# Kernel optimization log

Hardware: AMD Instinct MI355X
Metric: run time of the kernel (lower is better)

The kernel has to match this reference:

```python
import jax, jax.numpy as jnp
import numpy as np

N = 100000      # nodes
E = 3200000     # edges
F_IN = 78       # num_features_mol
F_GAT = 256     # mol_out_feats
HEADS = 2
F_HYP = 128     # mol_out_feats_hyper


def setup_inputs() -> dict:
    key = jax.random.key(0)
    ks = jax.random.split(key, 32)
    g = lambda k, s: jax.random.normal(k, s, dtype=jnp.float32) * 0.05
    inp = {}
    inp["mol_x"] = jax.random.normal(ks[0], (N, F_IN), dtype=jnp.float32)
    inp["mol_edge_index"] = jax.random.randint(ks[1], (2, E), 0, N)
    inp["hyper_edge"] = jax.random.randint(ks[2], (2, E), 0, N)
    # GAT layer 1 (78 -> 256, 2 heads, concat=False)
    inp["W1"] = g(ks[3], (F_IN, HEADS * F_GAT)); inp["as1"] = g(ks[4], (HEADS, F_GAT)); inp["ad1"] = g(ks[5], (HEADS, F_GAT)); inp["b1"] = jnp.zeros((F_GAT,), jnp.float32)
    # GAT layers 2,3 (256 -> 256)
    inp["W2"] = g(ks[6], (F_GAT, HEADS * F_GAT)); inp["as2"] = g(ks[7], (HEADS, F_GAT)); inp["ad2"] = g(ks[8], (HEADS, F_GAT)); inp["b2"] = jnp.zeros((F_GAT,), jnp.float32)
    inp["W3"] = g(ks[9], (F_GAT, HEADS * F_GAT)); inp["as3"] = g(ks[10], (HEADS, F_GAT)); inp["ad3"] = g(ks[11], (HEADS, F_GAT)); inp["b3"] = jnp.zeros((F_GAT,), jnp.float32)
    # GRU-style gating fusion
    inp["fc1_w"] = g(ks[12], (F_GAT, F_GAT)); inp["fc1_b"] = jnp.zeros((F_GAT,), jnp.float32)
    inp["fc2_w"] = g(ks[13], (F_GAT, F_GAT)); inp["fc2_b"] = jnp.zeros((F_GAT,), jnp.float32)
    inp["mol_bias"] = jax.random.uniform(ks[14], (1, F_GAT), jnp.float32, -0.2, 0.2)
    # HypergraphConv layers (334 -> 128 -> 128)
    inp["theta1"] = g(ks[15], (F_GAT + F_IN, F_HYP)); inp["hb1"] = jnp.zeros((F_HYP,), jnp.float32)
    inp["theta2"] = g(ks[16], (F_HYP, F_HYP)); inp["hb2"] = jnp.zeros((F_HYP,), jnp.float32)
    return inp


def _gat(x, src, dst, W, a_s, a_d, b):
    # PyG GATConv, heads=2, concat=False, eval mode (no dropout), self-loops pre-added in src/dst
    xh = (x @ W).reshape(N, HEADS, F_GAT)            # [N,H,C]
    a_src = (xh * a_s).sum(-1)                        # [N,H]
    a_dst = (xh * a_d).sum(-1)                        # [N,H]
    e = jax.nn.leaky_relu(a_src[src] + a_dst[dst], 0.2)  # [E',H]
    m = jax.ops.segment_max(e, dst, num_segments=N)
    ex = jnp.exp(e - m[dst])
    s = jax.ops.segment_sum(ex, dst, num_segments=N)
    alpha = ex / s[dst]                               # softmax over incoming edges
    out = jax.ops.segment_sum(xh[src] * alpha[:, :, None], dst, num_segments=N)
    return out.mean(axis=1) + b                       # concat=False -> head mean


def _hyper(x, node, edge, theta, b):
    # PyG HypergraphConv, use_attention=False: D^-1 H B^-1 H^T X Theta + b
    xt = x @ theta
    ones = jnp.ones((node.shape[0],), xt.dtype)
    D = jax.ops.segment_sum(ones, node, num_segments=N)
    B = jax.ops.segment_sum(ones, edge, num_segments=N)
    Dinv = jnp.where(D > 0, 1.0 / D, 0.0)
    Binv = jnp.where(B > 0, 1.0 / B, 0.0)
    ef = Binv[:, None] * jax.ops.segment_sum(xt[node], edge, num_segments=N)
    nf = Dinv[:, None] * jax.ops.segment_sum(ef[edge], node, num_segments=N)
    return nf + b


def _forward(mol_x, mol_edge_index, hyper_edge,
             W1, as1, ad1, b1, W2, as2, ad2, b2, W3, as3, ad3, b3,
             fc1_w, fc1_b, fc2_w, fc2_b, mol_bias, theta1, hb1, theta2, hb2):
    loops = jnp.arange(N, dtype=mol_edge_index.dtype)
    src = jnp.concatenate([mol_edge_index[0], loops])
    dst = jnp.concatenate([mol_edge_index[1], loops])
    hyper_x0 = jax.lax.stop_gradient(mol_x)  # .clone().detach()
    # layer 0
    h = jax.nn.relu(_gat(mol_x, src, dst, W1, as1, ad1, b1))
    # layer 1 (relu) + gate
    x = jax.nn.relu(_gat(h, src, dst, W2, as2, ad2, b2))
    z = jax.nn.sigmoid(x @ fc1_w.T + fc1_b + h @ fc2_w.T + fc2_b + mol_bias)
    h = z * x + (1.0 - z) * h
    # layer 2 (no relu) + gate
    x = _gat(h, src, dst, W3, as3, ad3, b3)
    z = jax.nn.sigmoid(x @ fc1_w.T + fc1_b + h @ fc2_w.T + fc2_b + mol_bias)
    h = z * x + (1.0 - z) * h
    # hypergraph branch (source uses mol_edge_index here, hyper_edge is unused)
    hx = jnp.concatenate([jax.lax.stop_gradient(h), hyper_x0], axis=1)
    node, edge = mol_edge_index[0], mol_edge_index[1]
    hx = jax.nn.relu(_hyper(hx, node, edge, theta1, hb1))
    hx = jax.nn.relu(_hyper(hx, node, edge, theta2, hb2))
    return jnp.concatenate([h, hx], axis=1)  # [N, 384]


def reference(mol_x, mol_edge_index, hyper_edge,
              W1, as1, ad1, b1, W2, as2, ad2, b2, W3, as3, ad3, b3,
              fc1_w, fc1_b, fc2_w, fc2_b, mol_bias, theta1, hb1, theta2, hb2):
    return _forward(mol_x, mol_edge_index, hyper_edge,
                    W1, as1, ad1, b1, W2, as2, ad2, b2, W3, as3, ad3, b3,
                    fc1_w, fc1_b, fc2_w, fc2_b, mol_bias, theta1, hb1, theta2, hb2)
```

## Files before the change

### kernel.cpp

```cpp
#include <hip/hip_runtime.h>

typedef unsigned short u16;
typedef __attribute__((ext_vector_type(8))) short short8v;
typedef __attribute__((ext_vector_type(8))) unsigned short ushort8v;
typedef __attribute__((ext_vector_type(4))) unsigned short ushort4v;
typedef __attribute__((ext_vector_type(4))) float f32x4;
typedef __attribute__((ext_vector_type(2))) float f32x2;

__device__ __forceinline__ float bf2f(u16 u) {
    union { unsigned int i; float f; } v; v.i = ((unsigned int)u) << 16; return v.f;
}
__device__ __forceinline__ u16 f2bf(float f) {
    union { float f; unsigned int i; } v; v.f = f;
    unsigned int i = v.i;
    return (u16)((i + 0x7FFFu + ((i >> 16) & 1u)) >> 16);
}
__device__ __forceinline__ float leaky02(float x) { return x > 0.f ? x : 0.2f * x; }
__device__ __forceinline__ float load_in(const void* p, long i, int isbf) {
    return isbf ? bf2f(((const u16*)p)[i]) : ((const float*)p)[i];
}
__device__ __forceinline__ f32x2 pk_fma(f32x2 a, f32x2 b, f32x2 c) {
    f32x2 d;
    asm("v_pk_fma_f32 %0, %1, %2, %3" : "=v"(d) : "v"(a), "v"(b), "v"(c));
    return d;
}
__device__ __forceinline__ f32x2 pk_add(f32x2 a, f32x2 b) {
    f32x2 d;
    asm("v_pk_add_f32 %0, %1, %2" : "=v"(d) : "v"(a), "v"(b));
    return d;
}
__device__ __forceinline__ f32x2 bfpair(unsigned int d) {
    union { unsigned int i; float f; } lo, hi;
    lo.i = d << 16;
    hi.i = d & 0xFFFF0000u;
    f32x2 r; r.x = lo.f; r.y = hi.f; return r;
}
__device__ __forceinline__ float bperm_f(int addr, float v) {
    return __int_as_float(__builtin_amdgcn_ds_bpermute(addr, __float_as_int(v)));
}
__device__ __forceinline__ int bperm_i(int addr, int v) {
    return __builtin_amdgcn_ds_bpermute(addr, v);
}

__global__ void detect_kernel(const unsigned* __restrict__ w, int* __restrict__ flag) {
    __shared__ int cnt;
    int t = threadIdx.x;
    if (t == 0) cnt = 0;
    __syncthreads();
    unsigned x = w[t * 16];
    unsigned lo = x & 0xFFFFu;
    int e = (int)((x >> 7) & 0xFFu);
    int good = (lo == 0u) || (e >= 100 && e <= 140);
    atomicAdd(&cnt, good);
    __syncthreads();
    if (t == 0) *flag = (cnt > 128) ? 1 : 0;
}

#define CSR_NBK 1024

__global__ __launch_bounds__(256)
void bucket_count_kernel(const int* __restrict__ ei, int* __restrict__ bcs,
                         int* __restrict__ bcd, int E_, int n, int SH) {
    __shared__ int hs[CSR_NBK], hd[CSR_NBK];
    const int t = threadIdx.x;
    for (int i = t; i < CSR_NBK; i += 256) { hs[i] = 0; hd[i] = 0; }
    __syncthreads();
    const int e0 = blockIdx.x * 4096;
    #pragma unroll
    for (int k = 0; k < 16; ++k) {
        int e = e0 + k * 256 + t;
        if (e < E_) {
            int s = ei[e], d = ei[E_ + e];
            if ((unsigned)s >= (unsigned)n) s = 0;
            if ((unsigned)d >= (unsigned)n) d = 0;
            atomicAdd(&hs[s >> SH], 1);
            atomicAdd(&hd[d >> SH], 1);
        }
    }
    __syncthreads();
    for (int i = t; i < CSR_NBK; i += 256) {
        if (hs[i]) atomicAdd(&bcs[i], hs[i]);
        if (hd[i]) atomicAdd(&bcd[i], hd[i]);
    }
}

__global__ void scan_excl_kernel(const int* __restrict__ deg, int* __restrict__ ptr, int n) {
    __shared__ int s_woff[17];
    __shared__ int s_carry;
    const int t = threadIdx.x;
    const int lane = t & 63, wid = t >> 6;
    if (t == 0) s_carry = 0;
    __syncthreads();
    for (int base = 0; base < n; base += 1024) {
        int i = base + t;
        int v = (i < n) ? deg[i] : 0;
        int incl = v;
        #pragma unroll
        for (int d = 1; d < 64; d <<= 1) {
            int x = __shfl_up(incl, d, 64);
            if (lane >= d) incl += x;
        }
        if (lane == 63) s_woff[wid] = incl;
        __syncthreads();
        if (t == 0) {
            int run = 0;
            #pragma unroll
            for (int w = 0; w < 16; ++w) { int x = s_woff[w]; s_woff[w] = run; run += x; }
            s_woff[16] = run;
        }
        __syncthreads();
        int excl = s_carry + s_woff[wid] + incl - v;
        if (i < n) ptr[i] = excl;
        __syncthreads();
        if (t == 0) s_carry += s_woff[16];
        __syncthreads();
    }
    if (t == 0) ptr[n] = s_carry;
}

__global__ void copy2_kernel(const int* __restrict__ a, int* __restrict__ b,
                             const int* __restrict__ c, int* __restrict__ d2, int n) {
    int i = blockIdx.x * 256 + threadIdx.x;
    if (i < n) { b[i] = a[i]; d2[i] = c[i]; }
}

__global__ __launch_bounds__(256)
void partition_kernel(const int* __restrict__ ei, int* __restrict__ bcur_s,
                      int* __restrict__ bcur_d, int2* __restrict__ ps,
                      int2* __restrict__ pd, int E_, int n, int SH) {
    __shared__ int cs[CSR_NBK], cd[CSR_NBK], bs[CSR_NBK], bd[CSR_NBK];
    const int t = threadIdx.x;
    for (int i = t; i < CSR_NBK; i += 256) { cs[i] = 0; cd[i] = 0; }
    __syncthreads();
    const int e0 = blockIdx.x * 4096;
    int sv[16], dv[16];
    #pragma unroll
    for (int k = 0; k < 16; ++k) {
        int e = e0 + k * 256 + t;
        int s = -1, d = 0;
        if (e < E_) {
            s = ei[e]; d = ei[E_ + e];
            if ((unsigned)s >= (unsigned)n) s = 0;
            if ((unsigned)d >= (unsigned)n) d = 0;
            atomicAdd(&cs[s >> SH], 1);
            atomicAdd(&cd[d >> SH], 1);
        }
        sv[k] = (e < E_) ? s : -1;
        dv[k] = d;
    }
    __syncthreads();
    for (int i = t; i < CSR_NBK; i += 256) {
        bs[i] = cs[i] ? atomicAdd(&bcur_s[i], cs[i]) : 0;
        bd[i] = cd[i] ? atomicAdd(&bcur_d[i], cd[i]) : 0;
        cs[i] = 0; cd[i] = 0;
    }
    __syncthreads();
    #pragma unroll
    for (int k = 0; k < 16; ++k) {
        int s = sv[k];
        if (s < 0) continue;
        int d = dv[k];
        int p = bs[s >> SH] + atomicAdd(&cs[s >> SH], 1);
        ps[p] = make_int2(d, s);
        int q = bd[d >> SH] + atomicAdd(&cd[d >> SH], 1);
        pd[q] = make_int2(s, d);
    }
}

__global__ __launch_bounds__(256)
void fill_bucket_kernel(const int2* __restrict__ pairs, const int* __restrict__ bptr,
                        int* __restrict__ ptr, int* __restrict__ idx, int n, int SH) {
    __shared__ int cnt[256];
    __shared__ int wsum[5];
    const int b = blockIdx.x;
    const int n0 = b << SH;
    if (n0 >= n) return;
    const int nn = min(1 << SH, n - n0);
    const int t = threadIdx.x;
    cnt[t] = 0;
    __syncthreads();
    const int pbeg = bptr[b], pend = bptr[b + 1];
    for (int j = pbeg + t; j < pend; j += 256)
        atomicAdd(&cnt[pairs[j].y - n0], 1);
    __syncthreads();
    const int c = (t < nn) ? cnt[t] : 0;
    int v = c;
    const int lane = t & 63, wid = t >> 6;
    #pragma unroll
    for (int d = 1; d < 64; d <<= 1) {
        int x = __shfl_up(v, d, 64);
        if (lane >= d) v += x;
    }
    if (lane == 63) wsum[wid] = v;
    __syncthreads();
    if (t == 0) {
        int r = 0;
        #pragma unroll
        for (int w = 0; w < 4; ++w) { int x = wsum[w]; wsum[w] = r; r += x; }
        wsum[4] = r;
    }
    __syncthreads();
    v += wsum[wid];
    const int excl = pbeg + v - c;
    __syncthreads();
    if (t < nn) { cnt[t] = excl; ptr[n0 + t] = excl; }
    if (t == 0 && n0 + nn == n) ptr[n] = pbeg + wsum[4];
    __syncthreads();
    for (int j = pbeg + t; j < pend; j += 256) {
        int2 pr = pairs[j];
        int p = atomicAdd(&cnt[pr.y - n0], 1);
        idx[p] = pr.x;
    }
}

__global__ void ingest_transpose_kernel(const void* __restrict__ src, long base,
                                        u16* __restrict__ dst, int K, int Nc, int Kp,
                                        const int* __restrict__ flag) {
    int i = blockIdx.x * 256 + threadIdx.x;
    if (i >= Nc * Kp) return;
    int n = i / Kp, k = i - n * Kp;
    float v = (k < K) ? load_in(src, base + (long)k * Nc + n, *flag) : 0.f;
    dst[i] = f2bf(v);
}

__global__ void ingest_copy_kernel(const void* __restrict__ src, u16* __restrict__ dst,
                                   int n, const int* __restrict__ flag) {
    int i = blockIdx.x * 256 + threadIdx.x;
    if (i < n) dst[i] = f2bf(load_in(src, i, *flag));
}

__global__ void ingest_wcat_kernel(const void* __restrict__ W, u16* __restrict__ dst,
                                   int Kin, int Fh, const int* __restrict__ flag) {
    int i = blockIdx.x * 256 + threadIdx.x;
    int tot = 256 * 2 * Fh;
    if (i >= tot) return;
    int o = i / (2 * Fh), k = i - o * 2 * Fh;
    int h = k / Fh, c = k - h * Fh;
    float v = (c < Kin) ? 0.5f * load_in(W, (long)c * 512 + h * 256 + o, *flag) : 0.f;
    dst[i] = f2bf(v);
}

__global__ void ingest_bcat_kernel(const void* __restrict__ fc1, const void* __restrict__ fc2,
                                   u16* __restrict__ dst, const int* __restrict__ flag) {
    int i = blockIdx.x * 256 + threadIdx.x;
    if (i >= 256 * 512) return;
    int o = i >> 9, k = i & 511;
    float v = (k < 256) ? load_in(fc1, (long)o * 256 + k, *flag)
                        : load_in(fc2, (long)o * 256 + k - 256, *flag);
    dst[i] = f2bf(v);
}

__global__ void ingest_pad_molx_kernel(const void* __restrict__ x, u16* __restrict__ dst,
                                       int ldd, int total, const int* __restrict__ flag) {
    int i = blockIdx.x * 256 + threadIdx.x;
    if (i >= total) return;
    int r = i / 96, c = i - r * 96;
    float v = (c < 78) ? load_in(x, (long)r * 78 + c, *flag) : 0.f;
    dst[(size_t)r * ldd + c] = f2bf(v);
}

__global__ void attn_vec_kernel(const void* __restrict__ W, const void* __restrict__ as_,
                                const void* __restrict__ ad_, float* __restrict__ was,
                                float* __restrict__ wad, int Kin, int Fh,
                                const int* __restrict__ flag) {
    int i = blockIdx.x * 256 + threadIdx.x;
    if (i >= 2 * Fh) return;
    int h = i / Fh, c = i - h * Fh;
    float s = 0.f, d = 0.f;
    if (c < Kin) {
        int f = *flag;
        for (int o = 0; o < 256; ++o) {
            float w = load_in(W, (long)c * 512 + h * 256 + o, f);
            s += w * load_in(as_, h * 256 + o, f);
            d += w * load_in(ad_, h * 256 + o, f);
        }
    }
    was[i] = s; wad[i] = d;
}

__global__ __launch_bounds__(256, 2)
void gemm_kernel(const u16* __restrict__ A, int lda,
                 const u16* __restrict__ Bt, int ldb,
                 u16* __restrict__ C, int ldc, int K, int M, int beta,
                 const u16* __restrict__ bias, int relu) {
    __shared__ __align__(16) u16 As[128 * 32];
    __shared__ __align__(16) u16 Bs[128 * 32];
    const int tid = threadIdx.x;
    const int wave = tid >> 6, lane = tid & 63;
    const int m0 = blockIdx.x * 128;
    const int n0 = blockIdx.y * 128;
    const int wm = (wave & 1) * 64, wn = (wave >> 1) * 64;
    const int r = lane & 15, q = lane >> 4;

    f32x4 acc[4][4];
    if (beta) {
        #pragma unroll
        for (int i = 0; i < 4; ++i)
            #pragma unroll
            for (int j = 0; j < 4; ++j)
                #pragma unroll
                for (int rr = 0; rr < 4; ++rr) {
                    size_t gr = (size_t)(m0 + wm + 16 * i + q * 4 + rr);
                    int gc = n0 + wn + 16 * j + r;
                    acc[i][j][rr] = bf2f(C[gr * ldc + gc]);
                }
    } else {
        #pragma unroll
        for (int i = 0; i < 4; ++i)
            #pragma unroll
            for (int j = 0; j < 4; ++j) acc[i][j] = (f32x4)0.f;
    }

    const int rowT = wave * 16 + (lane >> 2);
    const int koff = (lane & 3) * 8;
    int rA0 = m0 + rowT;       if (rA0 > M - 1) rA0 = M - 1;
    int rA1 = m0 + rowT + 64;  if (rA1 > M - 1) rA1 = M - 1;
    const u16* gA0 = A + (size_t)rA0 * lda + koff;
    const u16* gA1 = A + (size_t)rA1 * lda + koff;
    const u16* gB0 = Bt + (size_t)(n0 + rowT) * ldb + koff;
    const u16* gB1 = Bt + (size_t)(n0 + rowT + 64) * ldb + koff;
    u16* sA0 = &As[rowT * 32 + koff];
    u16* sA1 = &As[(rowT + 64) * 32 + koff];
    u16* sB0 = &Bs[rowT * 32 + koff];
    u16* sB1 = &Bs[(rowT + 64) * 32 + koff];

    const int nK = K >> 5;
    for (int kt = 0; kt < nK; ++kt) {
        ushort8v ta0 = *(const ushort8v*)gA0;
        ushort8v ta1 = *(const ushort8v*)gA1;
        ushort8v tb0 = *(const ushort8v*)gB0;
        ushort8v tb1 = *(const ushort8v*)gB1;
        gA0 += 32; gA1 += 32; gB0 += 32; gB1 += 32;
        __syncthreads();
        *(ushort8v*)sA0 = ta0;
        *(ushort8v*)sA1 = ta1;
        *(ushort8v*)sB0 = tb0;
        *(ushort8v*)sB1 = tb1;
        __syncthreads();
        short8v af[4], bf[4];
        #pragma unroll
        for (int i = 0; i < 4; ++i) af[i] = *(const short8v*)&As[(wm + 16 * i + r) * 32 + q * 8];
        #pragma unroll
        for (int j = 0; j < 4; ++j) bf[j] = *(const short8v*)&Bs[(wn + 16 * j + r) * 32 + q * 8];
        #pragma unroll
        for (int i = 0; i < 4; ++i)
            #pragma unroll
            for (int j = 0; j < 4; ++j)
                acc[i][j] = __builtin_amdgcn_mfma_f32_16x16x32_bf16(af[i], bf[j], acc[i][j], 0, 0, 0);
    }
    #pragma unroll
    for (int j = 0; j < 4; ++j) {
        int gc = n0 + wn + 16 * j + r;
        float bv = bias ? bf2f(bias[gc]) : 0.f;
        #pragma unroll
        for (int i = 0; i < 4; ++i)
            #pragma unroll
            for (int rr = 0; rr < 4; ++rr) {
                size_t gr = (size_t)(m0 + wm + 16 * i + q * 4 + rr);
                float x = acc[i][j][rr] + bv;
                if (relu) x = fmaxf(x, 0.f);
                C[gr * ldc + gc] = f2bf(x);
            }
    }
}

__global__ __launch_bounds__(256)
void attn_dots_h_kernel(const u16* __restrict__ hsrc, int ldh,
                        const float* __restrict__ was, const float* __restrict__ wad,
                        float* __restrict__ a_src, float* __restrict__ a_dst,
                        int Fh, int n) {
    int v = blockIdx.x * 4 + (threadIdx.x >> 6);
    if (v >= n) return;
    const int lane = threadIdx.x & 63;
    const int c0 = lane * 4;
    float ps0 = 0.f, pd0 = 0.f, ps1 = 0.f, pd1 = 0.f;
    if (c0 < Fh) {
        ushort4v xv = *(const ushort4v*)&hsrc[(size_t)v * ldh + c0];
        #pragma unroll
        for (int k = 0; k < 4; ++k) {
            float x = bf2f(xv[k]);
            ps0 += x * was[c0 + k];
            pd0 += x * wad[c0 + k];
            ps1 += x * was[Fh + c0 + k];
            pd1 += x * wad[Fh + c0 + k];
        }
    }
    #pragma unroll
    for (int d = 1; d < 64; d <<= 1) {
        ps0 += __shfl_xor(ps0, d, 64); pd0 += __shfl_xor(pd0, d, 64);
        ps1 += __shfl_xor(ps1, d, 64); pd1 += __shfl_xor(pd1, d, 64);
    }
    if (lane == 0) {
        a_src[2 * v] = ps0; a_src[2 * v + 1] = ps1;
        a_dst[2 * v] = pd0; a_dst[2 * v + 1] = pd1;
    }
}

template <int NG>
__global__ __launch_bounds__(256)
void gat_agg_h_kernel(const u16* __restrict__ hsrc, int ldh, int F,
                      const float* __restrict__ asrc, const float* __restrict__ adst,
                      const int* __restrict__ ptr, const int* __restrict__ idx,
                      u16* __restrict__ agg, int ldagg, int n, int Etot) {
    constexpr int GL = 64 / NG;
    int v = blockIdx.x * 4 + (threadIdx.x >> 6);
    if (v >= n) return;
    const int lane = threadIdx.x & 63;
    const int sub = lane / GL;
    const int c0 = (lane & (GL - 1)) * 8;
    const int act = (c0 < F);
    int beg = ptr[v], end = ptr[v + 1];
    beg = min(max(beg, 0), Etot);
    end = min(max(end, beg), Etot);
    const float ad0 = adst[2 * v], ad1 = adst[2 * v + 1];
    const float es0 = leaky02(asrc[2 * v] + ad0);
    const float es1 = leaky02(asrc[2 * v + 1] + ad1);
    float m0 = es0, m1 = es1;
    float s0 = 0.f, s1 = 0.f;
    f32x2 f0p[4], f1p[4];
    #pragma unroll
    for (int p = 0; p < 4; ++p) { f0p[p] = (f32x2)0.f; f1p[p] = (f32x2)0.f; }

    for (int cb = beg; cb < end; cb += 64) {
        const int cnt = min(64, end - cb);
        int sE = 0;
        float sc0 = -1e30f, sc1 = -1e30f;
        if (lane < cnt) {
            sE = idx[cb + lane];
            sE = ((unsigned)sE < (unsigned)n) ? sE : 0;
            sc0 = leaky02(asrc[2 * sE] + ad0);
            sc1 = leaky02(asrc[2 * sE + 1] + ad1);
        }
        float cm0 = sc0, cm1 = sc1;
        #pragma unroll
        for (int d = 1; d < 64; d <<= 1) {
            cm0 = fmaxf(cm0, __shfl_xor(cm0, d, 64));
            cm1 = fmaxf(cm1, __shfl_xor(cm1, d, 64));
        }
        const float nm0 = fmaxf(m0, cm0), nm1 = fmaxf(m1, cm1);
        const float r0 = __expf(m0 - nm0), r1 = __expf(m1 - nm1);
        m0 = nm0; m1 = nm1;
        s0 *= r0; s1 *= r1;
        #pragma unroll
        for (int p = 0; p < 4; ++p) {
            f0p[p].x *= r0; f0p[p].y *= r0;
            f1p[p].x *= r1; f1p[p].y *= r1;
        }
        float wE0 = 0.f, wE1 = 0.f;
        if (lane < cnt) {
            wE0 = __expf(sc0 - m0);
            wE1 = __expf(sc1 - m1);
            s0 += wE0; s1 += wE1;
        }
        const int nIt = (cnt + 4 * NG - 1) / (4 * NG);
        int jj = sub;
        for (int it = 0; it < nIt; ++it, jj += 4 * NG) {
            const int aA = jj * 4, aB = aA + NG * 4, aC = aA + NG * 8, aD = aA + NG * 12;
            const int sA = bperm_i(aA, sE);
            const int sB = bperm_i(aB, sE);
            const int sC = bperm_i(aC, sE);
            const int sD = bperm_i(aD, sE);
            const float wA0 = bperm_f(aA, wE0), wA1 = bperm_f(aA, wE1);
            const float wB0 = bperm_f(aB, wE0), wB1 = bperm_f(aB, wE1);
            const float wC0 = bperm_f(aC, wE0), wC1 = bperm_f(aC, wE1);
            const float wD0 = bperm_f(aD, wE0), wD1 = bperm_f(aD, wE1);
            if (act) {
                const uint4 fA = *(const uint4*)&hsrc[(size_t)sA * ldh + c0];
                const uint4 fB = *(const uint4*)&hsrc[(size_t)sB * ldh + c0];
                const uint4 fC = *(const uint4*)&hsrc[(size_t)sC * ldh + c0];
                const uint4 fD = *(const uint4*)&hsrc[(size_t)sD * ldh + c0];
                const f32x2 wA0v = {wA0, wA0}, wA1v = {wA1, wA1};
                const f32x2 wB0v = {wB0, wB0}, wB1v = {wB1, wB1};
                const f32x2 wC0v = {wC0, wC0}, wC1v = {wC1, wC1};
                const f32x2 wD0v = {wD0, wD0}, wD1v = {wD1, wD1};
                #pragma unroll
                for (int p = 0; p < 4; ++p) {
                    const f32x2 xA = bfpair(((const unsigned*)&fA)[p]);
                    const f32x2 xB = bfpair(((const unsigned*)&fB)[p]);
                    const f32x2 xC = bfpair(((const unsigned*)&fC)[p]);
                    const f32x2 xD = bfpair(((const unsigned*)&fD)[p]);
                    f0p[p] = pk_fma(xA, wA0v, f0p[p]);
                    f1p[p] = pk_fma(xA, wA1v, f1p[p]);
                    f0p[p] = pk_fma(xB, wB0v, f0p[p]);
                    f1p[p] = pk_fma(xB, wB1v, f1p[p]);
                    f0p[p] = pk_fma(xC, wC0v, f0p[p]);
                    f1p[p] = pk_fma(xC, wC1v, f1p[p]);
                    f0p[p] = pk_fma(xD, wD0v, f0p[p]);
                    f1p[p] = pk_fma(xD, wD1v, f1p[p]);
                }
            }
        }
    }
    #pragma unroll
    for (int d = 1; d < 64; d <<= 1) {
        s0 += __shfl_xor(s0, d, 64);
        s1 += __shfl_xor(s1, d, 64);
    }
    const float w0s = __expf(es0 - m0), w1s = __expf(es1 - m1);
    s0 += w0s; s1 += w1s;
    if (sub == 0 && act) {
        const uint4 f = *(const uint4*)&hsrc[(size_t)v * ldh + c0];
        const f32x2 w0v = {w0s, w0s}, w1v = {w1s, w1s};
        #pragma unroll
        for (int p = 0; p < 4; ++p) {
            const f32x2 x = bfpair(((const unsigned*)&f)[p]);
            f0p[p] = pk_fma(x, w0v, f0p[p]);
            f1p[p] = pk_fma(x, w1v, f1p[p]);
        }
    }
    #pragma unroll
    for (int p = 0; p < 4; ++p) {
        #pragma unroll
        for (int d = GL; d < 64; d <<= 1) {
            f0p[p].x += __shfl_xor(f0p[p].x, d, 64);
            f0p[p].y += __shfl_xor(f0p[p].y, d, 64);
            f1p[p].x += __shfl_xor(f1p[p].x, d, 64);
            f1p[p].y += __shfl_xor(f1p[p].y, d, 64);
        }
    }
    if (lane < GL && act) {
        const float i0 = 1.f / s0, i1 = 1.f / s1;
        ushort8v o0, o1;
        #pragma unroll
        for (int p = 0; p < 4; ++p) {
            o0[2 * p] = f2bf(f0p[p].x * i0); o0[2 * p + 1] = f2bf(f0p[p].y * i0);
            o1[2 * p] = f2bf(f1p[p].x * i1); o1[2 * p + 1] = f2bf(f1p[p].y * i1);
        }
        *(ushort8v*)&agg[(size_t)v * ldagg + c0] = o0;
        *(ushort8v*)&agg[(size_t)v * ldagg + F + c0] = o1;
    }
}

__global__ __launch_bounds__(256)
void gate_kernel(const u16* __restrict__ logit, const u16* __restrict__ cat,
                 const u16* __restrict__ fc1b, const u16* __restrict__ fc2b,
                 const u16* __restrict__ molb, u16* __restrict__ dest,
                 void* __restrict__ outw, const int* __restrict__ flag, int n) {
    int i = blockIdx.x * 256 + threadIdx.x;
    if (i >= n) return;
    int node = i >> 5, c0 = (i & 31) * 8;
    ushort8v lg = *(const ushort8v*)&logit[(size_t)node * 256 + c0];
    ushort8v xv = *(const ushort8v*)&cat[(size_t)node * 512 + c0];
    ushort8v hv = *(const ushort8v*)&cat[(size_t)node * 512 + 256 + c0];
    ushort8v b1v = *(const ushort8v*)&fc1b[c0];
    ushort8v b2v = *(const ushort8v*)&fc2b[c0];
    ushort8v mbv = *(const ushort8v*)&molb[c0];
    float ov[8];
    ushort8v dv;
    #pragma unroll
    for (int k = 0; k < 8; ++k) {
        float l = bf2f(lg[k]) + bf2f(b1v[k]) + bf2f(b2v[k]) + bf2f(mbv[k]);
        float z = 1.f / (1.f + __expf(-l));
        ov[k] = z * bf2f(xv[k]) + (1.f - z) * bf2f(hv[k]);
        dv[k] = f2bf(ov[k]);
    }
    *(ushort8v*)&dest[(size_t)node * 512 + c0] = dv;
    if (outw) {
        if (*flag) {
            *(ushort8v*)((u16*)outw + (size_t)node * 384 + c0) = dv;
        } else {
            float* o = (float*)outw + (size_t)node * 384 + c0;
            #pragma unroll
            for (int k = 0; k < 8; ++k) o[k] = ov[k];
        }
    }
}

__global__ __launch_bounds__(256)
void hyper_gather_kernel(const u16* __restrict__ feat, const int* __restrict__ ptr,
                         const int* __restrict__ idx, const u16* __restrict__ bias,
                         u16* __restrict__ outb, int ldo, void* __restrict__ outw,
                         int col0, const int* __restrict__ flag,
                         int do_relu, int n, int Etot) {
    int v = blockIdx.x * 4 + (threadIdx.x >> 6);
    if (v >= n) return;
    const int lane = threadIdx.x & 63;
    const int c0 = (lane & 15) * 8, sub = lane >> 4;
    int beg = ptr[v], end = ptr[v + 1];
    beg = min(max(beg, 0), Etot);
    end = min(max(end, beg), Etot);
    const float inv = (end > beg) ? 1.f / (float)(end - beg) : 0.f;
    f32x2 a2[4];
    #pragma unroll
    for (int p = 0; p < 4; ++p) a2[p] = (f32x2)0.f;
    int j = beg + sub;
    for (; j + 12 < end; j += 16) {
        int sA = idx[j];      sA = ((unsigned)sA < (unsigned)n) ? sA : 0;
        int sB = idx[j + 4];  sB = ((unsigned)sB < (unsigned)n) ? sB : 0;
        int sC = idx[j + 8];  sC = ((unsigned)sC < (unsigned)n) ? sC : 0;
        int sD = idx[j + 12]; sD = ((unsigned)sD < (unsigned)n) ? sD : 0;
        const uint4 fA = *(const uint4*)&feat[(size_t)sA * 128 + c0];
        const uint4 fB = *(const uint4*)&feat[(size_t)sB * 128 + c0];
        const uint4 fC = *(const uint4*)&feat[(size_t)sC * 128 + c0];
        const uint4 fD = *(const uint4*)&feat[(size_t)sD * 128 + c0];
        #pragma unroll
        for (int p = 0; p < 4; ++p) {
            a2[p] = pk_add(a2[p], bfpair(((const unsigned*)&fA)[p]));
            a2[p] = pk_add(a2[p], bfpair(((const unsigned*)&fB)[p]));
            a2[p] = pk_add(a2[p], bfpair(((const unsigned*)&fC)[p]));
            a2[p] = pk_add(a2[p], bfpair(((const unsigned*)&fD)[p]));
        }
    }
    for (; j < end; j += 4) {
        int s = idx[j]; s = ((unsigned)s < (unsigned)n) ? s : 0;
        const uint4 f = *(const uint4*)&feat[(size_t)s * 128 + c0];
        #pragma unroll
        for (int p = 0; p < 4; ++p)
            a2[p] = pk_add(a2[p], bfpair(((const unsigned*)&f)[p]));
    }
    #pragma unroll
    for (int p = 0; p < 4; ++p) {
        a2[p].x += __shfl_xor(a2[p].x, 16, 64);
        a2[p].y += __shfl_xor(a2[p].y, 16, 64);
        a2[p].x += __shfl_xor(a2[p].x, 32, 64);
        a2[p].y += __shfl_xor(a2[p].y, 32, 64);
    }
    if (sub == 0) {
        float ov[8];
        ushort8v o;
        #pragma unroll
        for (int p = 0; p < 4; ++p) {
            float x0 = a2[p].x * inv + (bias ? bf2f(bias[c0 + 2 * p]) : 0.f);
            float x1 = a2[p].y * inv + (bias ? bf2f(bias[c0 + 2 * p + 1]) : 0.f);
            if (do_relu) { x0 = fmaxf(x0, 0.f); x1 = fmaxf(x1, 0.f); }
            ov[2 * p] = x0; ov[2 * p + 1] = x1;
            o[2 * p] = f2bf(x0); o[2 * p + 1] = f2bf(x1);
        }
        if (outb) *(ushort8v*)&outb[(size_t)v * ldo + c0] = o;
        if (outw) {
            if (*flag) {
                *(ushort8v*)((u16*)outw + (size_t)v * 384 + col0 + c0) = o;
            } else {
                float* ofp = (float*)outw + (size_t)v * 384 + col0 + c0;
                #pragma unroll
                for (int k = 0; k < 8; ++k) ofp[k] = ov[k];
            }
        }
    }
}

extern "C" void kernel_launch(void* const* d_in, const int* in_sizes, int n_in,
                              void* d_out, int out_size, void* d_ws, size_t ws_size,
                              hipStream_t stream) {
    const void* molx = d_in[0];
    const int*  ei   = (const int*)d_in[1];
    const void* W1 = d_in[3], *as1 = d_in[4], *ad1 = d_in[5], *b1 = d_in[6];
    const void* W2 = d_in[7], *as2 = d_in[8], *ad2 = d_in[9], *b2 = d_in[10];
    const void* W3 = d_in[11], *as3 = d_in[12], *ad3 = d_in[13], *b3 = d_in[14];
    const void* fc1w = d_in[15], *fc1b = d_in[16], *fc2w = d_in[17], *fc2b = d_in[18];
    const void* molb = d_in[19];
    const void* th1 = d_in[20], *hb1 = d_in[21], *th2 = d_in[22], *hb2 = d_in[23];
    (void)n_in; (void)out_size;

    const int N = in_sizes[0] / 78;
    const int E = in_sizes[1] / 2;
    const int Mp = ((N + 127) / 128) * 128;

    int SH = 0;
    while (((N - 1) >> SH) >= CSR_NBK) SH++;

    char* base = (char*)d_ws;
    size_t off = 0;
    auto alloc = [&](size_t bytes) -> void* {
        void* r = base + off;
        off = (off + bytes + 255) & ~(size_t)255;
        return r;
    };
    int* flag = (int*)alloc(4);
    u16* bv1 = (u16*)alloc(256 * 2); u16* bv2 = (u16*)alloc(256 * 2); u16* bv3 = (u16*)alloc(256 * 2);
    u16* fc1bv = (u16*)alloc(256 * 2); u16* fc2bv = (u16*)alloc(256 * 2); u16* molbv = (u16*)alloc(256 * 2);
    u16* hb1v = (u16*)alloc(128 * 2); u16* hb2v = (u16*)alloc(128 * 2);
    float* was1 = (float*)alloc(192 * 4); float* wad1 = (float*)alloc(192 * 4);
    float* was2 = (float*)alloc(512 * 4); float* wad2 = (float*)alloc(512 * 4);
    float* was3 = (float*)alloc(512 * 4); float* wad3 = (float*)alloc(512 * 4);
    u16* Wc1 = (u16*)alloc(256 * 192 * 2);
    u16* Wc2 = (u16*)alloc(256 * 512 * 2);
    u16* Wc3 = (u16*)alloc(256 * 512 * 2);
    u16* Bcat = (u16*)alloc(256 * 512 * 2);
    u16* th1ta = (u16*)alloc(128 * 256 * 2);
    u16* th1tb = (u16*)alloc(128 * 96 * 2);
    u16* th2t  = (u16*)alloc(128 * 128 * 2);
    float* a_src = (float*)alloc((size_t)N * 2 * 4);
    float* a_dst = (float*)alloc((size_t)N * 2 * 4);
    int* ptr_src = (int*)alloc((size_t)(N + 1) * 4);
    int* ptr_dst = (int*)alloc((size_t)(N + 1) * 4);
    int* bcnt_src = (int*)alloc(CSR_NBK * 4);
    int* bcnt_dst = (int*)alloc(CSR_NBK * 4);
    int* bptr_src = (int*)alloc((CSR_NBK + 1) * 4);
    int* bptr_dst = (int*)alloc((CSR_NBK + 1) * 4);
    int* bcur_src = (int*)alloc(CSR_NBK * 4);
    int* bcur_dst = (int*)alloc(CSR_NBK * 4);
    int* idx_src = (int*)alloc((size_t)E * 4);
    int* idx_dst = (int*)alloc((size_t)E * 4);
    u16* cat = (u16*)alloc((size_t)Mp * 512 * 2);
    u16* agg = (u16*)alloc((size_t)Mp * 512 * 2);
    u16* xt   = agg;
    u16* efb  = agg + (size_t)Mp * 128;
    u16* hx1  = agg + (size_t)Mp * 256;
    u16* mxp2 = agg + (size_t)Mp * 384;

    int2* pairs_src; int2* pairs_dst;
    if (off + (size_t)E * 16 + 1024 <= ws_size) {
        pairs_src = (int2*)alloc((size_t)E * 8);
        pairs_dst = (int2*)alloc((size_t)E * 8);
    } else {
        pairs_src = (int2*)agg;
        pairs_dst = (int2*)((char*)agg + (size_t)E * 8);
    }

    const int nodeBlocks = (N + 3) / 4;
    const int eTiles = (E + 4095) / 4096;

    detect_kernel<<<1, 256, 0, stream>>>((const unsigned*)molx, flag);

    hipMemsetAsync(bcnt_src, 0, CSR_NBK * 4, stream);
    hipMemsetAsync(bcnt_dst, 0, CSR_NBK * 4, stream);
    bucket_count_kernel<<<eTiles, 256, 0, stream>>>(ei, bcnt_src, bcnt_dst, E, N, SH);
    scan_excl_kernel<<<1, 1024, 0, stream>>>(bcnt_src, bptr_src, CSR_NBK);
    scan_excl_kernel<<<1, 1024, 0, stream>>>(bcnt_dst, bptr_dst, CSR_NBK);
    copy2_kernel<<<(CSR_NBK + 255) / 256, 256, 0, stream>>>(bptr_src, bcur_src, bptr_dst, bcur_dst, CSR_NBK);
    partition_kernel<<<eTiles, 256, 0, stream>>>(ei, bcur_src, bcur_dst,
                                                 pairs_src, pairs_dst, E, N, SH);
    fill_bucket_kernel<<<CSR_NBK, 256, 0, stream>>>(pairs_src, bptr_src, ptr_src, idx_src, N, SH);
    fill_bucket_kernel<<<CSR_NBK, 256, 0, stream>>>(pairs_dst, bptr_dst, ptr_dst, idx_dst, N, SH);

    ingest_wcat_kernel<<<(256 * 192 + 255) / 256, 256, 0, stream>>>(W1, Wc1, 78, 96, flag);
    ingest_wcat_kernel<<<(256 * 512 + 255) / 256, 256, 0, stream>>>(W2, Wc2, 256, 256, flag);
    ingest_wcat_kernel<<<(256 * 512 + 255) / 256, 256, 0, stream>>>(W3, Wc3, 256, 256, flag);
    ingest_bcat_kernel<<<(256 * 512 + 255) / 256, 256, 0, stream>>>(fc1w, fc2w, Bcat, flag);
    ingest_transpose_kernel<<<(128 * 256 + 255) / 256, 256, 0, stream>>>(th1, 0, th1ta, 256, 128, 256, flag);
    ingest_transpose_kernel<<<(128 * 96 + 255) / 256, 256, 0, stream>>>(th1, (long)256 * 128, th1tb, 78, 128, 96, flag);
    ingest_transpose_kernel<<<(128 * 128 + 255) / 256, 256, 0, stream>>>(th2, 0, th2t, 128, 128, 128, flag);
    attn_vec_kernel<<<1, 256, 0, stream>>>(W1, as1, ad1, was1, wad1, 78, 96, flag);
    attn_vec_kernel<<<2, 256, 0, stream>>>(W2, as2, ad2, was2, wad2, 256, 256, flag);
    attn_vec_kernel<<<2, 256, 0, stream>>>(W3, as3, ad3, was3, wad3, 256, 256, flag);
    ingest_copy_kernel<<<1, 256, 0, stream>>>(b1, bv1, 256, flag);
    ingest_copy_kernel<<<1, 256, 0, stream>>>(b2, bv2, 256, flag);
    ingest_copy_kernel<<<1, 256, 0, stream>>>(b3, bv3, 256, flag);
    ingest_copy_kernel<<<1, 256, 0, stream>>>(fc1b, fc1bv, 256, flag);
    ingest_copy_kernel<<<1, 256, 0, stream>>>(fc2b, fc2bv, 256, flag);
    ingest_copy_kernel<<<1, 256, 0, stream>>>(molb, molbv, 256, flag);
    ingest_copy_kernel<<<1, 128, 0, stream>>>(hb1, hb1v, 128, flag);
    ingest_copy_kernel<<<1, 128, 0, stream>>>(hb2, hb2v, 128, flag);
    ingest_pad_molx_kernel<<<(N * 96 + 255) / 256, 256, 0, stream>>>(molx, cat, 512, N * 96, flag);

    auto gemm = [&](const u16* A, int lda, const u16* Bt, int ldb, u16* C, int ldc,
                    int K, int Nc, int M, int beta, const u16* bias, int relu) {
        dim3 g(Mp / 128, Nc / 128);
        gemm_kernel<<<g, 256, 0, stream>>>(A, lda, Bt, ldb, C, ldc, K, M, beta, bias, relu);
    };

    attn_dots_h_kernel<<<nodeBlocks, 256, 0, stream>>>(cat, 512, was1, wad1, a_src, a_dst, 96, N);
    gat_agg_h_kernel<4><<<nodeBlocks, 256, 0, stream>>>(cat, 512, 96, a_src, a_dst,
                                                        ptr_dst, idx_dst, agg, 192, N, E);
    gemm(agg, 192, Wc1, 192, cat + 256, 512, 192, 256, Mp, 0, bv1, 1);
    attn_dots_h_kernel<<<nodeBlocks, 256, 0, stream>>>(cat + 256, 512, was2, wad2, a_src, a_dst, 256, N);
    gat_agg_h_kernel<2><<<nodeBlocks, 256, 0, stream>>>(cat + 256, 512, 256, a_src, a_dst,
                                                        ptr_dst, idx_dst, agg, 512, N, E);
    gemm(agg, 512, Wc2, 512, cat, 512, 512, 256, Mp, 0, bv2, 1);
    gemm(cat, 512, Bcat, 512, agg , 256, 512, 256, Mp, 0, nullptr, 0);
    gate_kernel<<<(N * 32 + 255) / 256, 256, 0, stream>>>(agg, cat, fc1bv, fc2bv, molbv,
                                                          cat + 256, nullptr, flag, N * 32);
    attn_dots_h_kernel<<<nodeBlocks, 256, 0, stream>>>(cat + 256, 512, was3, wad3, a_src, a_dst, 256, N);
    gat_agg_h_kernel<2><<<nodeBlocks, 256, 0, stream>>>(cat + 256, 512, 256, a_src, a_dst,
                                                        ptr_dst, idx_dst, agg, 512, N, E);
    gemm(agg, 512, Wc3, 512, cat, 512, 512, 256, Mp, 0, bv3, 0);
    gemm(cat, 512, Bcat, 512, agg , 256, 512, 256, Mp, 0, nullptr, 0);
    gate_kernel<<<(N * 32 + 255) / 256, 256, 0, stream>>>(agg, cat, fc1bv, fc2bv, molbv,
                                                          cat + 256, d_out, flag, N * 32);
    ingest_pad_molx_kernel<<<(N * 96 + 255) / 256, 256, 0, stream>>>(molx, mxp2, 96, N * 96, flag);
    gemm(cat + 256, 512, th1ta, 256, xt, 128, 256, 128, Mp, 0, nullptr, 0);
    gemm(mxp2, 96, th1tb, 96, xt, 128, 96, 128, Mp, 1, nullptr, 0);
    hyper_gather_kernel<<<nodeBlocks, 256, 0, stream>>>(xt, ptr_dst, idx_dst, (const u16*)nullptr,
                                                        efb, 128, nullptr, 0, flag, 0, N, E);
    hyper_gather_kernel<<<nodeBlocks, 256, 0, stream>>>(efb, ptr_src, idx_src, hb1v,
                                                        hx1, 128, nullptr, 0, flag, 1, N, E);
    gemm(hx1, 128, th2t, 128, xt, 128, 128, 128, Mp, 0, nullptr, 0);
    hyper_gather_kernel<<<nodeBlocks, 256, 0, stream>>>(xt, ptr_dst, idx_dst, (const u16*)nullptr,
                                                        efb, 128, nullptr, 0, flag, 0, N, E);
    hyper_gather_kernel<<<nodeBlocks, 256, 0, stream>>>(efb, ptr_src, idx_src, hb2v,
                                                        (u16*)nullptr, 0, d_out, 256, flag, 1, N, E);
}
```

Measured before the change: 2.128 ms.

## Drop online-max softmax in GAT aggregation, use direct global-to-LDS GEMM loads

The GAT aggregation kernel drops the chunked online-softmax and its wave-wide max reductions and bpermute broadcasts. Each lane group now loads its own edge indices and computes exp weights directly, with scores clamped at 80 so the exponential cannot overflow. The GEMM stages tiles through global_load_lds instead of going via registers, and eight tiny bias-ingest launches become one kernel. The clamp replaces the exact max subtraction, which could differ numerically if scores are ever large, and the GEMM keeps a single LDS buffer with two barriers per K step.

```diff
diff --git a/kernel.cpp b/kernel.cpp
--- a/kernel.cpp
+++ b/kernel.cpp
@@ -35,12 +35,9 @@
     hi.i = d & 0xFFFF0000u;
     f32x2 r; r.x = lo.f; r.y = hi.f; return r;
 }
-__device__ __forceinline__ float bperm_f(int addr, float v) {
-    return __int_as_float(__builtin_amdgcn_ds_bpermute(addr, __float_as_int(v)));
-}
-__device__ __forceinline__ int bperm_i(int addr, int v) {
-    return __builtin_amdgcn_ds_bpermute(addr, v);
-}
+#define GLD_LDS16(g, s) __builtin_amdgcn_global_load_lds( \
+    (const __attribute__((address_space(1))) void*)(g),   \
+    (__attribute__((address_space(3))) void*)(s), 16, 0, 0)
 
 __global__ void detect_kernel(const unsigned* __restrict__ w, int* __restrict__ flag) {
     __shared__ int cnt;
@@ -223,10 +220,20 @@
     dst[i] = f2bf(v);
 }
 
-__global__ void ingest_copy_kernel(const void* __restrict__ src, u16* __restrict__ dst,
-                                   int n, const int* __restrict__ flag) {
-    int i = blockIdx.x * 256 + threadIdx.x;
-    if (i < n) dst[i] = f2bf(load_in(src, i, *flag));
+__global__ void ingest_vecs_kernel(const void* __restrict__ s0, const void* __restrict__ s1,
+                                   const void* __restrict__ s2, const void* __restrict__ s3,
+                                   const void* __restrict__ s4, const void* __restrict__ s5,
+                                   const void* __restrict__ s6, const void* __restrict__ s7,
+                                   u16* __restrict__ d0, u16* __restrict__ d1,
+                                   u16* __restrict__ d2, u16* __restrict__ d3,
+                                   u16* __restrict__ d4, u16* __restrict__ d5,
+                                   u16* __restrict__ d6, u16* __restrict__ d7,
+                                   const int* __restrict__ flag) {
+    const void* srcs[8] = {s0, s1, s2, s3, s4, s5, s6, s7};
+    u16* dsts[8] = {d0, d1, d2, d3, d4, d5, d6, d7};
+    const int b = blockIdx.x, t = threadIdx.x;
+    const int nsz = (b < 6) ? 256 : 128;
+    if (t < nsz) dsts[b][t] = f2bf(load_in(srcs[b], t, *flag));
 }
 
 __global__ void ingest_wcat_kernel(const void* __restrict__ W, u16* __restrict__ dst,
@@ -326,16 +333,12 @@
 
     const int nK = K >> 5;
     for (int kt = 0; kt < nK; ++kt) {
-        ushort8v ta0 = *(const ushort8v*)gA0;
-        ushort8v ta1 = *(const ushort8v*)gA1;
-        ushort8v tb0 = *(const ushort8v*)gB0;
-        ushort8v tb1 = *(const ushort8v*)gB1;
+        __syncthreads();
+        GLD_LDS16(gA0, sA0);
+        GLD_LDS16(gA1, sA1);
+        GLD_LDS16(gB0, sB0);
+        GLD_LDS16(gB1, sB1);
         gA0 += 32; gA1 += 32; gB0 += 32; gB1 += 32;
-        __syncthreads();
-        *(ushort8v*)sA0 = ta0;
-        *(ushort8v*)sA1 = ta1;
-        *(ushort8v*)sB0 = tb0;
-        *(ushort8v*)sB1 = tb1;
         __syncthreads();
         short8v af[4], bf[4];
         #pragma unroll
@@ -398,10 +401,10 @@
 
 template <int NG>
 __global__ __launch_bounds__(256)
-void gat_agg_h_kernel(const u16* __restrict__ hsrc, int ldh, int F,
-                      const float* __restrict__ asrc, const float* __restrict__ adst,
-                      const int* __restrict__ ptr, const int* __restrict__ idx,
-                      u16* __restrict__ agg, int ldagg, int n, int Etot) {
+void gat_agg_kernel(const u16* __restrict__ hsrc, int ldh, int F,
+                    const float* __restrict__ asrc, const float* __restrict__ adst,
+                    const int* __restrict__ ptr, const int* __restrict__ idx,
+                    u16* __restrict__ agg, int ldagg, int n, int Etot) {
     constexpr int GL = 64 / NG;
     int v = blockIdx.x * 4 + (threadIdx.x >> 6);
     if (v >= n) return;
@@ -413,94 +416,86 @@
     beg = min(max(beg, 0), Etot);
     end = min(max(end, beg), Etot);
     const float ad0 = adst[2 * v], ad1 = adst[2 * v + 1];
-    const float es0 = leaky02(asrc[2 * v] + ad0);
-    const float es1 = leaky02(asrc[2 * v + 1] + ad1);
-    float m0 = es0, m1 = es1;
+    const float es0 = fminf(leaky02(asrc[2 * v] + ad0), 80.f);
+    const float es1 = fminf(leaky02(asrc[2 * v + 1] + ad1), 80.f);
+    f32x2 f0p[4], f1p[4];
+    #pragma unroll
+    for (int p = 0; p < 4; ++p) { f0p[p] = (f32x2)0.f; f1p[p] = (f32x2)0.f; }
     float s0 = 0.f, s1 = 0.f;
-    f32x2 f0p[4], f1p[4];
-    #pragma unroll
-    for (int p = 0; p < 4; ++p) { f0p[p] = (f32x2)0.f; f1p[p] = (f32x2)0.f; }
-
-    for (int cb = beg; cb < end; cb += 64) {
-        const int cnt = min(64, end - cb);
-        int sE = 0;
-        float sc0 = -1e30f, sc1 = -1e30f;
-        if (lane < cnt) {
-            sE = idx[cb + lane];
-            sE = ((unsigned)sE < (unsigned)n) ? sE : 0;
-            sc0 = leaky02(asrc[2 * sE] + ad0);
-            sc1 = leaky02(asrc[2 * sE + 1] + ad1);
-        }
-        float cm0 = sc0, cm1 = sc1;
-        #pragma unroll
-        for (int d = 1; d < 64; d <<= 1) {
-            cm0 = fmaxf(cm0, __shfl_xor(cm0, d, 64));
-            cm1 = fmaxf(cm1, __shfl_xor(cm1, d, 64));
-        }
-        const float nm0 = fmaxf(m0, cm0), nm1 = fmaxf(m1, cm1);
-        const float r0 = __expf(m0 - nm0), r1 = __expf(m1 - nm1);
-        m0 = nm0; m1 = nm1;
-        s0 *= r0; s1 *= r1;
-        #pragma unroll
-        for (int p = 0; p < 4; ++p) {
-            f0p[p].x *= r0; f0p[p].y *= r0;
-            f1p[p].x *= r1; f1p[p].y *= r1;
-        }
-        float wE0 = 0.f, wE1 = 0.f;
-        if (lane < cnt) {
-            wE0 = __expf(sc0 - m0);
-            wE1 = __expf(sc1 - m1);
-            s0 += wE0; s1 += wE1;
-        }
-        const int nIt = (cnt + 4 * NG - 1) / (4 * NG);
-        int jj = sub;
-        for (int it = 0; it < nIt; ++it, jj += 4 * NG) {
-            const int aA = jj * 4, aB = aA + NG * 4, aC = aA + NG * 8, aD = aA + NG * 12;
-            const int sA = bperm_i(aA, sE);
-            const int sB = bperm_i(aB, sE);
-            const int sC = bperm_i(aC, sE);
-            const int sD = bperm_i(aD, sE);
-            const float wA0 = bperm_f(aA, wE0), wA1 = bperm_f(aA, wE1);
-            const float wB0 = bperm_f(aB, wE0), wB1 = bperm_f(aB, wE1);
-            const float wC0 = bperm_f(aC, wE0), wC1 = bperm_f(aC, wE1);
-            const float wD0 = bperm_f(aD, wE0), wD1 = bperm_f(aD, wE1);
-            if (act) {
-                const uint4 fA = *(const uint4*)&hsrc[(size_t)sA * ldh + c0];
-                const uint4 fB = *(const uint4*)&hsrc[(size_t)sB * ldh + c0];
-                const uint4 fC = *(const uint4*)&hsrc[(size_t)sC * ldh + c0];
-                const uint4 fD = *(const uint4*)&hsrc[(size_t)sD * ldh + c0];
-                const f32x2 wA0v = {wA0, wA0}, wA1v = {wA1, wA1};
-                const f32x2 wB0v = {wB0, wB0}, wB1v = {wB1, wB1};
-                const f32x2 wC0v = {wC0, wC0}, wC1v = {wC1, wC1};
-                const f32x2 wD0v = {wD0, wD0}, wD1v = {wD1, wD1};
-                #pragma unroll
-                for (int p = 0; p < 4; ++p) {
-                    const f32x2 xA = bfpair(((const unsigned*)&fA)[p]);
-                    const f32x2 xB = bfpair(((const unsigned*)&fB)[p]);
-                    const f32x2 xC = bfpair(((const unsigned*)&fC)[p]);
-                    const f32x2 xD = bfpair(((const unsigned*)&fD)[p]);
-                    f0p[p] = pk_fma(xA, wA0v, f0p[p]);
-                    f1p[p] = pk_fma(xA, wA1v, f1p[p]);
-                    f0p[p] = pk_fma(xB, wB0v, f0p[p]);
-                    f1p[p] = pk_fma(xB, wB1v, f1p[p]);
-                    f0p[p] = pk_fma(xC, wC0v, f0p[p]);
-                    f1p[p] = pk_fma(xC, wC1v, f1p[p]);
-                    f0p[p] = pk_fma(xD, wD0v, f0p[p]);
-                    f1p[p] = pk_fma(xD, wD1v, f1p[p]);
-                }
+
+    int j = beg + sub;
+    for (; j + 3 * NG < end; j += 4 * NG) {
+        int sA = idx[j];          sA = ((unsigned)sA < (unsigned)n) ? sA : 0;
+        int sB = idx[j + NG];     sB = ((unsigned)sB < (unsigned)n) ? sB : 0;
+        int sC = idx[j + 2 * NG]; sC = ((unsigned)sC < (unsigned)n) ? sC : 0;
+        int sD = idx[j + 3 * NG]; sD = ((unsigned)sD < (unsigned)n) ? sD : 0;
+        const float2 aA = *(const float2*)&asrc[2 * sA];
+        const float2 aB = *(const float2*)&asrc[2 * sB];
+        const float2 aC = *(const float2*)&asrc[2 * sC];
+        const float2 aD = *(const float2*)&asrc[2 * sD];
+        const float wA0 = __expf(fminf(leaky02(aA.x + ad0), 80.f));
+        const float wA1 = __expf(fminf(leaky02(aA.y + ad1), 80.f));
+        const float wB0 = __expf(fminf(leaky02(aB.x + ad0), 80.f));
+        const float wB1 = __expf(fminf(leaky02(aB.y + ad1), 80.f));
+        const float wC0 = __expf(fminf(leaky02(aC.x + ad0), 80.f));
+        const float wC1 = __expf(fminf(leaky02(aC.y + ad1), 80.f));
+        const float wD0 = __expf(fminf(leaky02(aD.x + ad0), 80.f));
+        const float wD1 = __expf(fminf(leaky02(aD.y + ad1), 80.f));
+        s0 += (wA0 + wB0) + (wC0 + wD0);
+        s1 += (wA1 + wB1) + (wC1 + wD1);
+        if (act) {
+            const uint4 fA = *(const uint4*)&hsrc[(size_t)sA * ldh + c0];
+            const uint4 fB = *(const uint4*)&hsrc[(size_t)sB * ldh + c0];
+            const uint4 fC = *(const uint4*)&hsrc[(size_t)sC * ldh + c0];
+            const uint4 fD = *(const uint4*)&hsrc[(size_t)sD * ldh + c0];
+            const f32x2 wA0v = {wA0, wA0}, wA1v = {wA1, wA1};
+            const f32x2 wB0v = {wB0, wB0}, wB1v = {wB1, wB1};
+            const f32x2 wC0v = {wC0, wC0}, wC1v = {wC1, wC1};
+            const f32x2 wD0v = {wD0, wD0}, wD1v = {wD1, wD1};
+            #pragma unroll
+            for (int p = 0; p < 4; ++p) {
+                const f32x2 xA = bfpair(((const unsigned*)&fA)[p]);
+                const f32x2 xB = bfpair(((const unsigned*)&fB)[p]);
+                const f32x2 xC = bfpair(((const unsigned*)&fC)[p]);
+                const f32x2 xD = bfpair(((const unsigned*)&fD)[p]);
+                f0p[p] = pk_fma(xA, wA0v, f0p[p]);
+                f1p[p] = pk_fma(xA, wA1v, f1p[p]);
+                f0p[p] = pk_fma(xB, wB0v, f0p[p]);
+                f1p[p] = pk_fma(xB, wB1v, f1p[p]);
+                f0p[p] = pk_fma(xC, wC0v, f0p[p]);
+                f1p[p] = pk_fma(xC, wC1v, f1p[p]);
+                f0p[p] = pk_fma(xD, wD0v, f0p[p]);
+                f1p[p] = pk_fma(xD, wD1v, f1p[p]);
             }
         }
     }
-    #pragma unroll
-    for (int d = 1; d < 64; d <<= 1) {
+    for (; j < end; j += NG) {
+        int sA = idx[j]; sA = ((unsigned)sA < (unsigned)n) ? sA : 0;
+        const float2 aA = *(const float2*)&asrc[2 * sA];
+        const float wA0 = __expf(fminf(leaky02(aA.x + ad0), 80.f));
+        const float wA1 = __expf(fminf(leaky02(aA.y + ad1), 80.f));
+        s0 += wA0; s1 += wA1;
+        if (act) {
+            const uint4 fA = *(const uint4*)&hsrc[(size_t)sA * ldh + c0];
+            const f32x2 wA0v = {wA0, wA0}, wA1v = {wA1, wA1};
+            #pragma unroll
+            for (int p = 0; p < 4; ++p) {
+                const f32x2 xA = bfpair(((const unsigned*)&fA)[p]);
+                f0p[p] = pk_fma(xA, wA0v, f0p[p]);
+                f1p[p] = pk_fma(xA, wA1v, f1p[p]);
+            }
+        }
+    }
+    #pragma unroll
+    for (int d = GL; d < 64; d <<= 1) {
         s0 += __shfl_xor(s0, d, 64);
         s1 += __shfl_xor(s1, d, 64);
     }
-    const float w0s = __expf(es0 - m0), w1s = __expf(es1 - m1);
-    s0 += w0s; s1 += w1s;
+    const float ws0 = __expf(es0), ws1 = __expf(es1);
+    s0 += ws0; s1 += ws1;
     if (sub == 0 && act) {
         const uint4 f = *(const uint4*)&hsrc[(size_t)v * ldh + c0];
-        const f32x2 w0v = {w0s, w0s}, w1v = {w1s, w1s};
+        const f32x2 w0v = {ws0, ws0}, w1v = {ws1, ws1};
         #pragma unroll
         for (int p = 0; p < 4; ++p) {
             const f32x2 x = bfpair(((const unsigned*)&f)[p]);
@@ -734,14 +729,9 @@
     attn_vec_kernel<<<1, 256, 0, stream>>>(W1, as1, ad1, was1, wad1, 78, 96, flag);
     attn_vec_kernel<<<2, 256, 0, stream>>>(W2, as2, ad2, was2, wad2, 256, 256, flag);
     attn_vec_kernel<<<2, 256, 0, stream>>>(W3, as3, ad3, was3, wad3, 256, 256, flag);
-    ingest_copy_kernel<<<1, 256, 0, stream>>>(b1, bv1, 256, flag);
-    ingest_copy_kernel<<<1, 256, 0, stream>>>(b2, bv2, 256, flag);
-    ingest_copy_kernel<<<1, 256, 0, stream>>>(b3, bv3, 256, flag);
-    ingest_copy_kernel<<<1, 256, 0, stream>>>(fc1b, fc1bv, 256, flag);
-    ingest_copy_kernel<<<1, 256, 0, stream>>>(fc2b, fc2bv, 256, flag);
-    ingest_copy_kernel<<<1, 256, 0, stream>>>(molb, molbv, 256, flag);
-    ingest_copy_kernel<<<1, 128, 0, stream>>>(hb1, hb1v, 128, flag);
-    ingest_copy_kernel<<<1, 128, 0, stream>>>(hb2, hb2v, 128, flag);
+    ingest_vecs_kernel<<<8, 256, 0, stream>>>(b1, b2, b3, fc1b, fc2b, molb, hb1, hb2,
+                                              bv1, bv2, bv3, fc1bv, fc2bv, molbv,
+                                              hb1v, hb2v, flag);
     ingest_pad_molx_kernel<<<(N * 96 + 255) / 256, 256, 0, stream>>>(molx, cat, 512, N * 96, flag);
 
     auto gemm = [&](const u16* A, int lda, const u16* Bt, int ldb, u16* C, int ldc,
@@ -751,19 +741,19 @@
     };
 
     attn_dots_h_kernel<<<nodeBlocks, 256, 0, stream>>>(cat, 512, was1, wad1, a_src, a_dst, 96, N);
-    gat_agg_h_kernel<4><<<nodeBlocks, 256, 0, stream>>>(cat, 512, 96, a_src, a_dst,
-                                                        ptr_dst, idx_dst, agg, 192, N, E);
+    gat_agg_kernel<4><<<nodeBlocks, 256, 0, stream>>>(cat, 512, 96, a_src, a_dst,
+                                                      ptr_dst, idx_dst, agg, 192, N, E);
     gemm(agg, 192, Wc1, 192, cat + 256, 512, 192, 256, Mp, 0, bv1, 1);
     attn_dots_h_kernel<<<nodeBlocks, 256, 0, stream>>>(cat + 256, 512, was2, wad2, a_src, a_dst, 256, N);
-    gat_agg_h_kernel<2><<<nodeBlocks, 256, 0, stream>>>(cat + 256, 512, 256, a_src, a_dst,
-                                                        ptr_dst, idx_dst, agg, 512, N, E);
+    gat_agg_kernel<2><<<nodeBlocks, 256, 0, stream>>>(cat + 256, 512, 256, a_src, a_dst,
+                                                      ptr_dst, idx_dst, agg, 512, N, E);
     gemm(agg, 512, Wc2, 512, cat, 512, 512, 256, Mp, 0, bv2, 1);
     gemm(cat, 512, Bcat, 512, agg , 256, 512, 256, Mp, 0, nullptr, 0);
     gate_kernel<<<(N * 32 + 255) / 256, 256, 0, stream>>>(agg, cat, fc1bv, fc2bv, molbv,
                                                           cat + 256, nullptr, flag, N * 32);
     attn_dots_h_kernel<<<nodeBlocks, 256, 0, stream>>>(cat + 256, 512, was3, wad3, a_src, a_dst, 256, N);
-    gat_agg_h_kernel<2><<<nodeBlocks, 256, 0, stream>>>(cat + 256, 512, 256, a_src, a_dst,
-                                                        ptr_dst, idx_dst, agg, 512, N, E);
+    gat_agg_kernel<2><<<nodeBlocks, 256, 0, stream>>>(cat + 256, 512, 256, a_src, a_dst,
+                                                      ptr_dst, idx_dst, agg, 512, N, E);
     gemm(agg, 512, Wc3, 512, cat, 512, 512, 256, Mp, 0, bv3, 0);
     gemm(cat, 512, Bcat, 512, agg , 256, 512, 256, Mp, 0, nullptr, 0);
     gate_kernel<<<(N * 32 + 255) / 256, 256, 0, stream>>>(agg, cat, fc1bv, fc2bv, molbv,
```

New measurement: 2.155 ms. No clear change (+1.3%).
